# Optimization experiments

Hardware: AMD Instinct MI355X
Metric: run time of the kernel (lower is better)

## Reference

```python
import jax, jax.numpy as jnp
import numpy as np

HEADS = 8
EPS = 1e-5


def _quad_sums(a):
    """a: (B,h,H,W,...) -> (B,h,H,W,4,...) sums over the four inclusive
    quadrants [ :h+1,:w+1 | :h+1,w: | h:,:w+1 | h:,w: ] for every (h,w),
    via padded 2D prefix sums over axes (2,3)."""
    c = jnp.cumsum(jnp.cumsum(a, axis=2), axis=3)
    pads = [(0, 0)] * a.ndim
    pads[2] = (1, 0)
    pads[3] = (1, 0)
    P = jnp.pad(c, pads)  # P[...,i,j,...] = sum over rows<i, cols<j
    tl = P[:, :, 1:, 1:]
    tr = P[:, :, 1:, -1:] - P[:, :, 1:, :-1]
    bl = P[:, :, -1:, 1:] - P[:, :, :-1, 1:]
    br = P[:, :, -1:, -1:] - P[:, :, :-1, -1:] - P[:, :, -1:, :-1] + P[:, :, :-1, :-1]
    return jnp.stack([tl, tr, bl, br], axis=4)


def setup_inputs():
    key = jax.random.key(0)
    ks = jax.random.split(key, 12)
    B, H, W, D = 64, 48, 48, 64
    n = H * W
    hD = HEADS * D  # inner_dim = heads * dim_head, dim_head == dim
    rn = lambda k, shape: jax.random.normal(k, shape, dtype=jnp.float32) * 0.02
    return {
        "x": jax.random.normal(ks[0], (B, n, D), dtype=jnp.float32),
        "ln_g": jnp.ones((D,), jnp.float32),
        "ln_b": jnp.zeros((D,), jnp.float32),
        "Wqkv": rn(ks[1], (3 * hD, D)),
        "bqkv": jnp.zeros((3 * hD,), jnp.float32),
        "cls_tok": rn(ks[2], (D,)),
        "Wwqkv": rn(ks[3], (3 * D, D)),
        "bwqkv": jnp.zeros((3 * D,), jnp.float32),
        "Wwproj": rn(ks[4], (D, D)),
        "bwproj": jnp.zeros((D,), jnp.float32),
        "Wraq": rn(ks[5], (D, D)),
        "Wrak": rn(ks[6], (D, D)),
        "Wrav": rn(ks[7], (D, D)),
        "Wrao": rn(ks[8], (D, D)),
        "brao": jnp.zeros((D,), jnp.float32),
        "Wout": rn(ks[9], (D, hD)),
        "bout": jnp.zeros((D,), jnp.float32),
    }


def reference(x, ln_g, ln_b, Wqkv, bqkv, cls_tok, Wwqkv, bwqkv, Wwproj, bwproj,
              Wraq, Wrak, Wrav, Wrao, brao, Wout, bout):
    B, n, D = x.shape
    H = W = int(np.sqrt(n))
    h = HEADS
    hd = D // h                      # WindowAttention head dim
    scale_w = hd ** -0.5             # WindowAttention qk scale
    scale_ra = (D // h) ** -0.5      # RegionAggregator scale

    # LayerNorm (biased variance, as torch)
    mu = x.mean(-1, keepdims=True)
    var = ((x - mu) ** 2).mean(-1, keepdims=True)
    xn = (x - mu) / jnp.sqrt(var + EPS) * ln_g + ln_b

    # to_qkv: only q is consumed downstream (k, v are dead in the original forward)
    q = xn @ Wqkv[: h * D].T + bqkv[: h * D]
    q = q.reshape(B, n, h, D).transpose(0, 2, 1, 3)  # (B,h,n,D)  d == dim

    # WindowAttention: per-quadrant CLS-row attention, shared token keys/values.
    cls_qkv = (cls_tok @ Wwqkv.T + bwqkv).reshape(3, h, hd)
    q_c = cls_qkv[0] * scale_w                       # (h,hd) scaled cls query
    k_c, v_c = cls_qkv[1], cls_qkv[2]
    tok = (xn @ Wwqkv.T + bwqkv).reshape(B, n, 3, h, hd)
    k_t = tok[:, :, 1].transpose(0, 2, 1, 3)         # (B,h,n,hd)
    v_t = tok[:, :, 2].transpose(0, 2, 1, 3)
    logits = jnp.einsum('hd,bhnd->bhn', q_c, k_t)    # cls -> token logits
    cls_logit = jnp.einsum('hd,hd->h', q_c, k_c)     # cls -> cls logit
    m = jnp.maximum(logits.max(-1), cls_logit)       # (B,h) stabilizer
    e = jnp.exp(logits - m[..., None]).reshape(B, h, H, W)
    ecls = jnp.exp(cls_logit - m)                    # (B,h)
    ev = e[..., None] * v_t.reshape(B, h, H, W, hd)
    Se = _quad_sums(e)                               # (B,h,H,W,4)
    Sev = _quad_sums(ev)                             # (B,h,H,W,4,hd)
    denom = ecls[:, :, None, None, None] + Se
    num = ecls[:, :, None, None, None, None] * v_c[None, :, None, None, None, :] + Sev
    cls_out = num / denom[..., None]                 # (B,h,H,W,4,hd)
    cls_out = cls_out.transpose(0, 2, 3, 4, 1, 5).reshape(B, n, 4, D)
    regions = cls_out @ Wwproj.T + bwproj            # (B,n,4,D)

    # RegionAggregator (regions are identical across heads -> broadcast)
    qp = jnp.einsum('bhnd,ed->bhne', q, Wraq)
    kp = regions @ Wrak.T                            # (B,n,4,D)
    vp = regions @ Wrav.T
    scores = jnp.einsum('bhnd,bnrd->bhnr', qp, kp) * scale_ra
    attn = jax.nn.softmax(scores, axis=-1)
    agg = jnp.einsum('bhnr,bnrd->bhnd', attn, vp)
    out = agg @ Wrao.T + brao                        # (B,h,n,D)
    out = out.transpose(0, 2, 1, 3).reshape(B, n, h * D)
    return out @ Wout.T + bout                       # (B,n,D)
```

## Files before the change

kernel.cpp:

```cpp
#include <hip/hip_runtime.h>
#include <math.h>


#define SCALE_W  0.3535533905932738f
#define SCALE_RA 0.3535533905932738f
#define LN_EPS 1e-5f

typedef __attribute__((ext_vector_type(8))) short bf16x8;
typedef __attribute__((ext_vector_type(4))) float f32x4;

#define OFF_XN   0ull
#define SZ_XN    (64ull*2304*64)
#define OFF_KT   (OFF_XN + SZ_XN)
#define SZ_KT    (64ull*8*2304*8)
#define OFF_VT   (OFF_KT + SZ_KT)
#define OFF_PA   (OFF_VT + SZ_KT)
#define SZ_PA    (512ull*2401*5)
#define OFF_PB   (OFF_PA + SZ_PA)
#define SZ_PB    (512ull*2401*4)
#define OFF_ECLS (OFF_PB + SZ_PB)
#define OFF_QC   (OFF_ECLS + 512)
#define OFF_KC   (OFF_QC + 64)
#define OFF_VC   (OFF_KC + 64)
#define OFF_CLOG (OFF_VC + 64)
#define OFF_BK   (OFF_CLOG + 8)
#define OFF_BV   (OFF_BK + 64)
#define OFF_AH   (OFF_BV + 64)
#define OFF_W1   (OFF_AH + 512)
#define OFF_WZ   (OFF_W1 + 64)
#define OFF_B2   (OFF_WZ + 64)
#define OFF_V2   (OFF_B2 + 512)
#define OFF_UH   (OFF_V2 + 512)
#define OFF_CH   (OFF_UH + 512)
#define OFF_C1   (OFF_CH + 8)
#define OFF_G    (OFF_C1 + 64)
#define OFF_Z    (OFF_G + 32768)

__device__ inline void split2(float x, unsigned short &h, unsigned short &l) {
  unsigned u = __float_as_uint(x);
  unsigned hr = (u + 0x7fffu + ((u >> 16) & 1u)) >> 16;
  h = (unsigned short)hr;
  float hf = __uint_as_float(hr << 16);
  float lo = x - hf;
  unsigned u2 = __float_as_uint(lo);
  l = (unsigned short)((u2 + 0x7fffu + ((u2 >> 16) & 1u)) >> 16);
}

__device__ inline void split2x2(float x0, float x1, unsigned &h, unsigned &l) {
  asm("v_cvt_pk_bf16_f32 %0, %1, %2" : "=v"(h) : "v"(x0), "v"(x1));
  float r0 = x0 - __uint_as_float(h << 16);
  float r1 = x1 - __uint_as_float(h & 0xffff0000u);
  asm("v_cvt_pk_bf16_f32 %0, %1, %2" : "=v"(l) : "v"(r0), "v"(r1));
}

__device__ inline float dot64(const float* __restrict__ a, const float* __restrict__ b) {
  float s0 = 0.f, s1 = 0.f, s2 = 0.f, s3 = 0.f;
  #pragma unroll
  for (int d = 0; d < 64; d += 4) {
    float4 av = *(const float4*)(a + d);
    float4 bv = *(const float4*)(b + d);
    s0 += av.x * bv.x; s1 += av.y * bv.y;
    s2 += av.z * bv.z; s3 += av.w * bv.w;
  }
  return (s0 + s1) + (s2 + s3);
}

__global__ __launch_bounds__(256) void k_pre(const float* __restrict__ x,
      const float* __restrict__ ln_g, const float* __restrict__ ln_b,
      const float* __restrict__ Wqkv, const float* __restrict__ bqkv,
      const float* __restrict__ cls_tok, const float* __restrict__ Wwqkv,
      const float* __restrict__ bwqkv, const float* __restrict__ Wwproj,
      const float* __restrict__ bwproj, const float* __restrict__ Wraq,
      const float* __restrict__ Wrak, const float* __restrict__ Wrav,
      const float* __restrict__ Wrao, const float* __restrict__ brao,
      const float* __restrict__ Wout, const float* __restrict__ bout,
      float* __restrict__ ws) {
  __shared__ float smu[12928];
  int tid = threadIdx.x;
  int blk = blockIdx.x;

  if (blk < 2304) {
    float* xnT = smu;
    float* xt  = smu + 4352;
    float* wkv = smu + 4352;
    float* muL = smu + 4352 + 8448;
    float* rsL = muL + 64;

    long T0 = (long)blk * 64;
    int tok = tid >> 2, seg = tid & 3;

    const float4* x4 = (const float4*)(x + (T0 + tok)*64 + seg*16);
    float4 va = x4[0], vb = x4[1], vc4 = x4[2], vd = x4[3];
    {
      float* xp = xt + tok*65 + seg*16;
      xp[0]=va.x; xp[1]=va.y; xp[2]=va.z; xp[3]=va.w;
      xp[4]=vb.x; xp[5]=vb.y; xp[6]=vb.z; xp[7]=vb.w;
      xp[8]=vc4.x; xp[9]=vc4.y; xp[10]=vc4.z; xp[11]=vc4.w;
      xp[12]=vd.x; xp[13]=vd.y; xp[14]=vd.z; xp[15]=vd.w;
    }
    __syncthreads();
    if (tid < 64) {
      float s = 0.f;
      for (int i2 = 0; i2 < 64; ++i2) s += xt[tid*65 + i2];
      float mu = s * (1.0f/64.0f);
      float v = 0.f;
      for (int i2 = 0; i2 < 64; ++i2) { float d = xt[tid*65 + i2] - mu; v += d*d; }
      v *= (1.0f/64.0f);
      muL[tid] = mu; rsL[tid] = 1.0f / sqrtf(v + LN_EPS);
    }
    __syncthreads();
    {
      float mu = muL[tok], rs = rsL[tok];
      float xv[16];
      #pragma unroll
      for (int k = 0; k < 16; ++k) {
        int i2 = seg*16 + k;
        float v = (xt[tok*65 + i2] - mu) * rs * ln_g[i2] + ln_b[i2];
        xv[k] = v;
        xnT[i2*68 + tok] = v;
      }
      float4* xng = (float4*)(ws + OFF_XN + (T0 + tok)*64 + seg*16);
      xng[0] = make_float4(xv[0], xv[1], xv[2], xv[3]);
      xng[1] = make_float4(xv[4], xv[5], xv[6], xv[7]);
      xng[2] = make_float4(xv[8], xv[9], xv[10], xv[11]);
      xng[3] = make_float4(xv[12], xv[13], xv[14], xv[15]);
    }
    __syncthreads();
    {
      int o = tid >> 1, dh = (tid & 1) * 32;
      #pragma unroll
      for (int k = 0; k < 32; k += 4) {
        float4 w4 = *(const float4*)(Wwqkv + (64 + o)*64 + dh + k);
        wkv[(dh+k+0)*132 + o] = w4.x;
        wkv[(dh+k+1)*132 + o] = w4.y;
        wkv[(dh+k+2)*132 + o] = w4.z;
        wkv[(dh+k+3)*132 + o] = w4.w;
      }
    }
    __syncthreads();
    int tokq = tid & 15, og = tid >> 4;
    float acc[4][8];
    #pragma unroll
    for (int ti = 0; ti < 4; ++ti)
      #pragma unroll
      for (int k = 0; k < 8; ++k) acc[ti][k] = 0.f;
    for (int d2 = 0; d2 < 64; ++d2) {
      float4 a4 = *(float4*)&xnT[d2*68 + tokq*4];
      float4 b0 = *(float4*)&wkv[d2*132 + og*8];
      float4 b1 = *(float4*)&wkv[d2*132 + og*8 + 4];
      float aa[4] = {a4.x, a4.y, a4.z, a4.w};
      float bbv[8] = {b0.x,b0.y,b0.z,b0.w,b1.x,b1.y,b1.z,b1.w};
      #pragma unroll
      for (int ti = 0; ti < 4; ++ti)
        #pragma unroll
        for (int k = 0; k < 8; ++k) acc[ti][k] += aa[ti]*bbv[k];
    }
    int hh2 = og & 7;
    float bsv[8];
    #pragma unroll
    for (int k = 0; k < 8; ++k) bsv[k] = bwqkv[64 + og*8 + k];
    unsigned long long dstoff = (og < 8) ? OFF_KT : OFF_VT;
    #pragma unroll
    for (int ti = 0; ti < 4; ++ti) {
      long ntok = T0 + tokq*4 + ti;
      int bb = (int)(ntok / 2304);
      int nl = (int)(ntok % 2304);
      float* dst = ws + dstoff + ((long)(bb*8 + hh2)*2304 + nl)*8;
      *(float4*)dst = make_float4(acc[ti][0]+bsv[0], acc[ti][1]+bsv[1], acc[ti][2]+bsv[2], acc[ti][3]+bsv[3]);
      *(float4*)(dst+4) = make_float4(acc[ti][4]+bsv[4], acc[ti][5]+bsv[5], acc[ti][6]+bsv[6], acc[ti][7]+bsv[7]);
    }
  } else if (blk < 2320) {
    float* A  = smu;
    float* Bl = smu + 4160;
    int wblk = blk - 2304;
    if (wblk < 8) {
      int hh = wblk;
      for (int o = tid; o < 4096; o += 256) {
        int d = o & 63, e = o >> 6; float s = 0.f;
        for (int f = 0; f < 64; ++f) s += Wraq[f*64+d] * Wrak[f*64+e];
        A[d*65 + e] = s;
      }
      __syncthreads();
      for (int o = tid; o < 4096; o += 256) {
        int j = o & 63, i = o >> 6; float s = 0.f;
        for (int f = 0; f < 64; ++f) s += A[i*65 + f] * Wwproj[f*64 + j];
        Bl[i*65 + j] = s;
      }
      __syncthreads();
      unsigned short* gb = (unsigned short*)(ws + OFF_G) + hh*8192;
      for (int o = tid; o < 4096; o += 256) {
        int d = o & 63, e = o >> 6; float s = 0.f;
        for (int f = 0; f < 64; ++f) s += Wqkv[(hh*64+f)*64 + d] * Bl[f*65 + e];
        unsigned short h16, l16;
        split2(s, h16, l16);
        int base = (e >> 4)*2048 + (d >> 5)*1024 + (((d >> 3) & 3)*16 + (e & 15))*8 + (d & 7);
        gb[base]       = h16;
        gb[base + 512] = l16;
      }
    } else {
      int hh = wblk - 8;
      for (int o = tid; o < 4096; o += 256) {
        int d = o & 63, e = o >> 6; float s = 0.f;
        for (int f = 0; f < 64; ++f) s += Wrav[e*64+f] * Wwproj[f*64+d];
        A[e*65 + d] = s;
      }
      __syncthreads();
      for (int o = tid; o < 4096; o += 256) {
        int d = o & 63, i = o >> 6; float s = 0.f;
        for (int f = 0; f < 64; ++f) s += Wrao[i*64+f] * A[f*65 + d];
        Bl[i*65 + d] = s;
      }
      __syncthreads();
      unsigned short* zb = (unsigned short*)(ws + OFF_Z) + hh*8192;
      for (int o = tid; o < 4096; o += 256) {
        int d = o & 63, e = o >> 6; float s = 0.f;
        for (int f = 0; f < 64; ++f) s += Wout[e*512 + hh*64 + f] * Bl[f*65 + d];
        unsigned short h16, l16;
        split2(s, h16, l16);
        int base = (e >> 4)*2048 + (d >> 5)*1024 + (((d >> 3) & 3)*16 + (e & 15))*8 + (d & 7);
        zb[base]       = h16;
        zb[base + 512] = l16;
      }
    }
  } else {
    float* bwz = smu;
    for (int idx = tid; idx < 768; idx += 256) {
      if (idx < 192) {
        float s = bwqkv[idx] + dot64(Wwqkv + idx*64, cls_tok);
        if (idx < 64) ws[OFF_QC + idx] = s * SCALE_W;
        else if (idx < 128) ws[OFF_KC + idx - 64] = s;
        else ws[OFF_VC + idx - 128] = s;
      } else if (idx < 256) {
        int e = idx - 192;
        ws[OFF_BV + e] = dot64(Wrav + e*64, bwproj);
      } else {
        int t2 = idx - 256; int hh = t2 >> 6, e = t2 & 63;
        ws[OFF_AH + t2] = dot64(Wraq + e*64, bqkv + hh*64);
      }
    }
    __syncthreads();
    for (int idx = tid; idx < 584; idx += 256) {
      if (idx < 8) {
        float s = 0.f;
        for (int u = 0; u < 8; ++u) s += ws[OFF_QC + idx*8+u] * ws[OFF_KC + idx*8+u];
        ws[OFF_CLOG + idx] = s;
      } else if (idx < 72) {
        int e = idx - 8;
        ws[OFF_WZ + e] = dot64(Wrao + e*64, ws + OFF_BV);
      } else {
        int t2 = idx - 72; int hh = t2 >> 6, e = t2 & 63; float s = 0.f;
        for (int d = 0; d < 64; ++d) s += Wrak[d*64+e] * ws[OFF_AH + hh*64+d];
        ws[OFF_B2 + t2] = s;
      }
    }
    __syncthreads();
    if (tid < 64) bwz[tid] = brao[tid] + ws[OFF_WZ + tid];
    __syncthreads();
    for (int idx = tid; idx < 576; idx += 256) {
      if (idx < 512) {
        int hh = idx >> 6, e = idx & 63; float s = 0.f;
        for (int d = 0; d < 64; ++d) s += Wwproj[d*64+e] * ws[OFF_B2 + hh*64+d];
        ws[OFF_V2 + idx] = s;
      } else {
        int e = idx - 512;
        float s0 = 0.f, s1 = 0.f, s2 = 0.f, s3 = 0.f;
        for (int f = 0; f < 512; f += 4) {
          float4 w4 = *(const float4*)(Wout + e*512 + f);
          float4 b4 = *(const float4*)&bwz[f & 63];
          s0 += w4.x*b4.x; s1 += w4.y*b4.y; s2 += w4.z*b4.z; s3 += w4.w*b4.w;
        }
        ws[OFF_C1 + e] = bout[e] + (s0 + s1) + (s2 + s3);
      }
    }
  }
}

__global__ __launch_bounds__(512) void k_prefix(float* __restrict__ ws) {
  __shared__ float Pp[49*49*5];
  __shared__ float red[8];
  int tid = threadIdx.x;
  int blk = blockIdx.x;
  int g = blk & 1, bh = blk >> 1;
  int hh = bh & 7;
  const float* kt = ws + OFF_KT + (long)bh*2304*8;
  const float* vt = ws + OFF_VT + (long)bh*2304*8 + (g ? 4 : 0);
  float qc[8];
  #pragma unroll
  for (int u = 0; u < 8; ++u) qc[u] = ws[OFF_QC + hh*8 + u];
  float lgr[5];
  float mloc = -1e30f;
  #pragma unroll
  for (int it = 0; it < 5; ++it) {
    int nn = tid + it*512;
    if (nn < 2304) {
      const float4* kk = (const float4*)(kt + nn*8);
      float4 k0 = kk[0], k1 = kk[1];
      float lv = qc[0]*k0.x + qc[1]*k0.y + qc[2]*k0.z + qc[3]*k0.w
               + qc[4]*k1.x + qc[5]*k1.y + qc[6]*k1.z + qc[7]*k1.w;
      lgr[it] = lv;
      mloc = fmaxf(mloc, lv);
    }
  }
  #pragma unroll
  for (int mk = 1; mk < 64; mk <<= 1) mloc = fmaxf(mloc, __shfl_xor(mloc, mk, 64));
  if ((tid & 63) == 0) red[tid >> 6] = mloc;
  __syncthreads();
  float m = fmaxf(fmaxf(fmaxf(red[0], red[1]), fmaxf(red[2], red[3])),
                  fmaxf(fmaxf(red[4], red[5]), fmaxf(red[6], red[7])));
  m = fmaxf(m, ws[OFF_CLOG + hh]);
  if (tid == 0 && g == 0) ws[OFF_ECLS + bh] = __expf(ws[OFF_CLOG + hh] - m);
  #pragma unroll
  for (int it = 0; it < 5; ++it) {
    int nn = tid + it*512;
    if (nn < 2304) {
      int i2 = nn / 48, j2 = nn % 48;
      float ev = __expf(lgr[it] - m);
      float4 v4 = *(const float4*)(vt + nn*8);
      float* cell = &Pp[((i2+1)*49 + (j2+1))*5];
      if (g == 0) {
        cell[0] = ev; cell[1] = ev*v4.x; cell[2] = ev*v4.y; cell[3] = ev*v4.z; cell[4] = ev*v4.w;
      } else {
        cell[0] = ev*v4.x; cell[1] = ev*v4.y; cell[2] = ev*v4.z; cell[3] = ev*v4.w;
      }
    }
  }
  __syncthreads();
  int nc = g ? 4 : 5;
  if (tid < 48*nc) {
    int j2 = tid / nc + 1, c = tid % nc;
    float s = 0.f;
    for (int i0 = 1; i0 <= 48; i0 += 8) {
      float v[8];
      #pragma unroll
      for (int k = 0; k < 8; ++k) v[k] = Pp[((i0+k)*49 + j2)*5 + c];
      #pragma unroll
      for (int k = 0; k < 8; ++k) { s += v[k]; v[k] = s; }
      #pragma unroll
      for (int k = 0; k < 8; ++k) Pp[((i0+k)*49 + j2)*5 + c] = v[k];
    }
  }
  __syncthreads();
  if (tid < 48*nc) {
    int i2 = tid / nc + 1, c = tid % nc;
    float s = 0.f;
    for (int j0 = 1; j0 <= 48; j0 += 8) {
      float v[8];
      #pragma unroll
      for (int k = 0; k < 8; ++k) v[k] = Pp[(i2*49 + j0+k)*5 + c];
      #pragma unroll
      for (int k = 0; k < 8; ++k) { s += v[k]; v[k] = s; }
      #pragma unroll
      for (int k = 0; k < 8; ++k) Pp[(i2*49 + j0+k)*5 + c] = v[k];
    }
  }
  __syncthreads();
  if (g == 0) {
    float* pa = ws + OFF_PA + (long)bh*12005;
    for (int idx = tid; idx < 12005; idx += 512) {
      int cell = idx / 5;
      int ii = cell / 49, jj = cell % 49;
      pa[idx] = (ii && jj) ? Pp[idx] : 0.f;
    }
  } else {
    float* pb = ws + OFF_PB + (long)bh*9604;
    for (int idx = tid; idx < 9604; idx += 512) {
      int cell = idx >> 2, c = idx & 3;
      int ii = cell / 49, jj = cell % 49;
      pb[idx] = (ii && jj) ? Pp[cell*5 + c] : 0.f;
    }
  }
}

__global__ __launch_bounds__(128) void k_main(const float* __restrict__ ws,
                                              float* __restrict__ outp) {
  __shared__ __align__(16) unsigned short XNhi[16*64];
  __shared__ __align__(16) unsigned short XNlo[16*64];
  __shared__ __align__(16) unsigned short CBhi[16*128];
  __shared__ __align__(16) unsigned short CBlo[16*128];
  __shared__ __align__(16) float Tlds[16*128];

  int tid = threadIdx.x;
  int tok = tid >> 3, eg = tid & 7;
  int lane = tid & 63, wv = tid >> 6;
  int quad = lane >> 4, lrow = lane & 15;
  int wcol = wv;
  long T0 = (long)blockIdx.x * 16;
  int b = (int)(T0 / 2304);
  int n = (int)(T0 % 2304) + tok;
  int i2 = n / 48, j2 = n % 48;

  {
    const float4* p4 = (const float4*)(ws + OFF_XN + (T0 + tok)*64 + eg*8);
    float4 xa = p4[0], xb = p4[1];
    float xv[8] = {xa.x, xa.y, xa.z, xa.w, xb.x, xb.y, xb.z, xb.w};
    union { unsigned u[4]; uint2 d[2]; } ph, pl;
    #pragma unroll
    for (int k = 0; k < 8; k += 2) split2x2(xv[k], xv[k+1], ph.u[k>>1], pl.u[k>>1]);
    int off = tok*64 + ((eg*8) ^ ((tok & 7) << 3));
    *(uint2*)&XNhi[off]     = ph.d[0];
    *(uint2*)&XNhi[off + 4] = ph.d[1];
    *(uint2*)&XNlo[off]     = pl.d[0];
    *(uint2*)&XNlo[off + 4] = pl.d[1];
  }

  float cls0[8], cls1[8], cls2[8], cls3[8];
  {
    float ec = ws[OFF_ECLS + b*8 + eg];
    const float* PA = ws + OFF_PA + (long)(b*8 + eg)*12005;
    const float* PB = ws + OFF_PB + (long)(b*8 + eg)*9604;
    int c_ij  = i2*49 + j2;
    int c_ij1 = c_ij + 1;
    int c_iW  = i2*49 + 48;
    int c_1j  = c_ij + 49;
    int c_1j1 = c_1j + 1;
    int c_1W  = c_iW + 49;
    int c_Hj  = 48*49 + j2;
    int c_Hj1 = c_Hj + 1;
    int c_HW  = 48*49 + 48;
    float rden[4];
    {
      float tl = PA[c_1j1*5];
      float tr = PA[c_1W*5] - PA[c_1j*5];
      float bl = PA[c_Hj1*5] - PA[c_ij1*5];
      float br = PA[c_HW*5] - PA[c_iW*5] - PA[c_Hj*5] + PA[c_ij*5];
      rden[0] = 1.0f/(ec + tl); rden[1] = 1.0f/(ec + tr);
      rden[2] = 1.0f/(ec + bl); rden[3] = 1.0f/(ec + br);
    }
    #pragma unroll
    for (int u = 0; u < 4; ++u) {
      int c = 1 + u;
      float tl = PA[c_1j1*5 + c];
      float tr = PA[c_1W*5 + c] - PA[c_1j*5 + c];
      float bl = PA[c_Hj1*5 + c] - PA[c_ij1*5 + c];
      float br = PA[c_HW*5 + c] - PA[c_iW*5 + c] - PA[c_Hj*5 + c] + PA[c_ij*5 + c];
      float nv = ec * ws[OFF_VC + eg*8 + u];
      cls0[u] = (nv + tl) * rden[0];
      cls1[u] = (nv + tr) * rden[1];
      cls2[u] = (nv + bl) * rden[2];
      cls3[u] = (nv + br) * rden[3];
    }
    #pragma unroll
    for (int u = 4; u < 8; ++u) {
      int c = u - 4;
      float tl = PB[c_1j1*4 + c];
      float tr = PB[c_1W*4 + c] - PB[c_1j*4 + c];
      float bl = PB[c_Hj1*4 + c] - PB[c_ij1*4 + c];
      float br = PB[c_HW*4 + c] - PB[c_iW*4 + c] - PB[c_Hj*4 + c] + PB[c_ij*4 + c];
      float nv = ec * ws[OFF_VC + eg*8 + u];
      cls0[u] = (nv + tl) * rden[0];
      cls1[u] = (nv + tr) * rden[1];
      cls2[u] = (nv + bl) * rden[2];
      cls3[u] = (nv + br) * rden[3];
    }
  }
  __syncthreads();

  const unsigned short* gball = (const unsigned short*)(ws + OFF_G);
  const unsigned short* zball = (const unsigned short*)(ws + OFF_Z);

  f32x4 oa0 = {0.f,0.f,0.f,0.f};
  f32x4 oa1 = {0.f,0.f,0.f,0.f};

  int rr = lrow;
  int sw3 = (rr & 7) << 3;
  const unsigned short* arh = XNhi + rr*64;
  const unsigned short* arl = XNlo + rr*64;
  const unsigned short* crh = CBhi + rr*128;
  const unsigned short* crl = CBlo + rr*128;

  for (int it = 0; it < 4; ++it) {
    int h0 = it*2;
    {
      union { bf16x8 v; uint2 d[2]; } ah0, ah1, al0, al1;
      int oa = (quad*8) ^ sw3;
      int ob = (32 + quad*8) ^ sw3;
      ah0.d[0] = *(const uint2*)(arh + oa); ah0.d[1] = *(const uint2*)(arh + oa + 4);
      ah1.d[0] = *(const uint2*)(arh + ob); ah1.d[1] = *(const uint2*)(arh + ob + 4);
      al0.d[0] = *(const uint2*)(arl + oa); al0.d[1] = *(const uint2*)(arl + oa + 4);
      al1.d[0] = *(const uint2*)(arl + ob); al1.d[1] = *(const uint2*)(arl + ob + 4);
      #pragma unroll
      for (int c = 0; c < 4; ++c) {
        int colb = wcol*4 + c;
        int e0 = colb*16 + lrow;
        const unsigned short* gh = gball + (h0 + (colb >> 2))*8192 + (colb & 3)*2048 + lane*8;
        bf16x8 bh0 = *(const bf16x8*)(gh);
        bf16x8 bl0 = *(const bf16x8*)(gh + 512);
        bf16x8 bh1 = *(const bf16x8*)(gh + 1024);
        bf16x8 bl1 = *(const bf16x8*)(gh + 1536);
        f32x4 acc = {0.f,0.f,0.f,0.f};
        acc = __builtin_amdgcn_mfma_f32_16x16x32_bf16(ah0.v, bh0, acc, 0, 0, 0);
        acc = __builtin_amdgcn_mfma_f32_16x16x32_bf16(ah1.v, bh1, acc, 0, 0, 0);
        acc = __builtin_amdgcn_mfma_f32_16x16x32_bf16(al0.v, bh0, acc, 0, 0, 0);
        acc = __builtin_amdgcn_mfma_f32_16x16x32_bf16(al1.v, bh1, acc, 0, 0, 0);
        acc = __builtin_amdgcn_mfma_f32_16x16x32_bf16(ah0.v, bl0, acc, 0, 0, 0);
        acc = __builtin_amdgcn_mfma_f32_16x16x32_bf16(ah1.v, bl1, acc, 0, 0, 0);
        float v2v = ws[OFF_V2 + h0*64 + e0];
        #pragma unroll
        for (int r = 0; r < 4; ++r) {
          int trow = quad*4 + r;
          Tlds[trow*128 + (e0 ^ ((trow & 7) << 2))] = acc[r] + v2v;
        }
      }
    }
    __syncthreads();
    {
      float tv0[8], tv1[8];
      {
        int base = tok*128;
        int sw2 = (tok & 7) << 2;
        float4 a0 = *(const float4*)&Tlds[base + ((eg*8) ^ sw2)];
        float4 b0 = *(const float4*)&Tlds[base + ((eg*8 + 4) ^ sw2)];
        float4 a1 = *(const float4*)&Tlds[base + ((64 + eg*8) ^ sw2)];
        float4 b1 = *(const float4*)&Tlds[base + ((64 + eg*8 + 4) ^ sw2)];
        tv0[0]=a0.x; tv0[1]=a0.y; tv0[2]=a0.z; tv0[3]=a0.w;
        tv0[4]=b0.x; tv0[5]=b0.y; tv0[6]=b0.z; tv0[7]=b0.w;
        tv1[0]=a1.x; tv1[1]=a1.y; tv1[2]=a1.z; tv1[3]=a1.w;
        tv1[4]=b1.x; tv1[5]=b1.y; tv1[6]=b1.z; tv1[7]=b1.w;
      }
      float p0=0.f,p1=0.f,p2=0.f,p3=0.f,q0=0.f,q1=0.f,q2=0.f,q3=0.f;
      #pragma unroll
      for (int k = 0; k < 8; ++k) {
        p0 += tv0[k]*cls0[k]; p1 += tv0[k]*cls1[k];
        p2 += tv0[k]*cls2[k]; p3 += tv0[k]*cls3[k];
        q0 += tv1[k]*cls0[k]; q1 += tv1[k]*cls1[k];
        q2 += tv1[k]*cls2[k]; q3 += tv1[k]*cls3[k];
      }
      #pragma unroll
      for (int mk = 1; mk < 8; mk <<= 1) {
        p0 += __shfl_xor(p0, mk, 8); p1 += __shfl_xor(p1, mk, 8);
        p2 += __shfl_xor(p2, mk, 8); p3 += __shfl_xor(p3, mk, 8);
        q0 += __shfl_xor(q0, mk, 8); q1 += __shfl_xor(q1, mk, 8);
        q2 += __shfl_xor(q2, mk, 8); q3 += __shfl_xor(q3, mk, 8);
      }
      union { unsigned u[4]; uint2 d[2]; } ch, cl;
      int cbBase = tok*128;
      int swc = (tok & 7) << 3;
      {
        float s0 = p0*SCALE_RA, s1 = p1*SCALE_RA, s2 = p2*SCALE_RA, s3 = p3*SCALE_RA;
        float mm = fmaxf(fmaxf(s0, s1), fmaxf(s2, s3));
        float e0 = __expf(s0-mm), e1 = __expf(s1-mm), e2 = __expf(s2-mm), e3 = __expf(s3-mm);
        float inv = 1.0f/(e0+e1+e2+e3);
        float av0 = e0*inv, av1 = e1*inv, av2 = e2*inv, av3 = e3*inv;
        #pragma unroll
        for (int k = 0; k < 8; k += 2) {
          float cv0 = av0*cls0[k] + av1*cls1[k] + av2*cls2[k] + av3*cls3[k];
          float cv1 = av0*cls0[k+1] + av1*cls1[k+1] + av2*cls2[k+1] + av3*cls3[k+1];
          split2x2(cv0, cv1, ch.u[k>>1], cl.u[k>>1]);
        }
        int o = cbBase + ((eg*8) ^ swc);
        *(uint2*)&CBhi[o]     = ch.d[0]; *(uint2*)&CBhi[o + 4] = ch.d[1];
        *(uint2*)&CBlo[o]     = cl.d[0]; *(uint2*)&CBlo[o + 4] = cl.d[1];
      }
      {
        float s0 = q0*SCALE_RA, s1 = q1*SCALE_RA, s2 = q2*SCALE_RA, s3 = q3*SCALE_RA;
        float mm = fmaxf(fmaxf(s0, s1), fmaxf(s2, s3));
        float e0 = __expf(s0-mm), e1 = __expf(s1-mm), e2 = __expf(s2-mm), e3 = __expf(s3-mm);
        float inv = 1.0f/(e0+e1+e2+e3);
        float av0 = e0*inv, av1 = e1*inv, av2 = e2*inv, av3 = e3*inv;
        #pragma unroll
        for (int k = 0; k < 8; k += 2) {
          float cv0 = av0*cls0[k] + av1*cls1[k] + av2*cls2[k] + av3*cls3[k];
          float cv1 = av0*cls0[k+1] + av1*cls1[k+1] + av2*cls2[k+1] + av3*cls3[k+1];
          split2x2(cv0, cv1, ch.u[k>>1], cl.u[k>>1]);
        }
        int o = cbBase + ((64 + eg*8) ^ swc);
        *(uint2*)&CBhi[o]     = ch.d[0]; *(uint2*)&CBhi[o + 4] = ch.d[1];
        *(uint2*)&CBlo[o]     = cl.d[0]; *(uint2*)&CBlo[o + 4] = cl.d[1];
      }
    }
    __syncthreads();
    {
      #pragma unroll
      for (int c = 0; c < 2; ++c) {
        int colb = wcol*2 + c;
        int e0 = colb*16 + lrow;
        f32x4 acc = (c == 0) ? oa0 : oa1;
        #pragma unroll
        for (int kb = 0; kb < 4; ++kb) {
          union { bf16x8 v; uint2 d[2]; } ah, al;
          int o = (kb*32 + quad*8) ^ sw3;
          ah.d[0] = *(const uint2*)(crh + o); ah.d[1] = *(const uint2*)(crh + o + 4);
          al.d[0] = *(const uint2*)(crl + o); al.d[1] = *(const uint2*)(crl + o + 4);
          const unsigned short* zc = zball + (h0 + (kb >> 1))*8192 + colb*2048 + (kb & 1)*1024 + lane*8;
          bf16x8 bh = *(const bf16x8*)(zc);
          bf16x8 bl = *(const bf16x8*)(zc + 512);
          acc = __builtin_amdgcn_mfma_f32_16x16x32_bf16(ah.v, bh, acc, 0, 0, 0);
          acc = __builtin_amdgcn_mfma_f32_16x16x32_bf16(al.v, bh, acc, 0, 0, 0);
          acc = __builtin_amdgcn_mfma_f32_16x16x32_bf16(ah.v, bl, acc, 0, 0, 0);
        }
        if (c == 0) oa0 = acc; else oa1 = acc;
      }
    }
  }
  #pragma unroll
  for (int c = 0; c < 2; ++c) {
    int e0 = (wcol*2 + c)*16 + lrow;
    float cov = ws[OFF_C1 + e0];
    f32x4 oa = (c == 0) ? oa0 : oa1;
    #pragma unroll
    for (int r = 0; r < 4; ++r)
      outp[(T0 + quad*4 + r)*64 + e0] = oa[r] + cov;
  }
}

extern "C" void kernel_launch(void* const* d_in, const int* in_sizes, int n_in,
                              void* d_out, int out_size, void* d_ws, size_t ws_size,
                              hipStream_t stream) {
  const float* x      = (const float*)d_in[0];
  const float* ln_g   = (const float*)d_in[1];
  const float* ln_b   = (const float*)d_in[2];
  const float* Wqkv   = (const float*)d_in[3];
  const float* bqkv   = (const float*)d_in[4];
  const float* cls_tok= (const float*)d_in[5];
  const float* Wwqkv  = (const float*)d_in[6];
  const float* bwqkv  = (const float*)d_in[7];
  const float* Wwproj = (const float*)d_in[8];
  const float* bwproj = (const float*)d_in[9];
  const float* Wraq   = (const float*)d_in[10];
  const float* Wrak   = (const float*)d_in[11];
  const float* Wrav   = (const float*)d_in[12];
  const float* Wrao   = (const float*)d_in[13];
  const float* brao   = (const float*)d_in[14];
  const float* Wout   = (const float*)d_in[15];
  const float* bout   = (const float*)d_in[16];
  float* ws = (float*)d_ws;
  float* outp = (float*)d_out;

  hipLaunchKernelGGL(k_pre, dim3(2321), dim3(256), 0, stream,
                     x, ln_g, ln_b, Wqkv, bqkv, cls_tok, Wwqkv, bwqkv,
                     Wwproj, bwproj, Wraq, Wrak, Wrav, Wrao, brao, Wout, bout, ws);
  hipLaunchKernelGGL(k_prefix, dim3(1024), dim3(512), 0, stream, ws);
  hipLaunchKernelGGL(k_main, dim3(9216), dim3(128), 0, stream, ws, outp);
}
```

Baseline: 360.9 us.

## Merge prefix-sum block pairs and schedule weight-prep blocks first in k_pre

k_prefix used to launch two blocks per (batch, head), and each one recomputed the logits, max and exponentials. It now launches one block that computes them once and runs two passes through the shared-memory prefix-sum buffer: first e with ev[0..3], then ev[4..7]. k_pre block indices are remapped so the small weight-precompute blocks come first and no longer trail behind the 2304 token blocks. The cost is half as many k_prefix blocks, each with more serial work and extra barriers, which lowers parallelism on a large GPU.

```diff
diff --git a/kernel.cpp b/kernel.cpp
--- a/kernel.cpp
+++ b/kernel.cpp
@@ -79,14 +79,14 @@
   int tid = threadIdx.x;
   int blk = blockIdx.x;
 
-  if (blk < 2304) {
+  if (blk >= 17) {
     float* xnT = smu;
     float* xt  = smu + 4352;
     float* wkv = smu + 4352;
     float* muL = smu + 4352 + 8448;
     float* rsL = muL + 64;
 
-    long T0 = (long)blk * 64;
+    long T0 = (long)(blk - 17) * 64;
     int tok = tid >> 2, seg = tid & 3;
 
     const float4* x4 = (const float4*)(x + (T0 + tok)*64 + seg*16);
@@ -169,10 +169,10 @@
       *(float4*)dst = make_float4(acc[ti][0]+bsv[0], acc[ti][1]+bsv[1], acc[ti][2]+bsv[2], acc[ti][3]+bsv[3]);
       *(float4*)(dst+4) = make_float4(acc[ti][4]+bsv[4], acc[ti][5]+bsv[5], acc[ti][6]+bsv[6], acc[ti][7]+bsv[7]);
     }
-  } else if (blk < 2320) {
+  } else if (blk >= 1) {
     float* A  = smu;
     float* Bl = smu + 4160;
-    int wblk = blk - 2304;
+    int wblk = blk - 1;
     if (wblk < 8) {
       int hh = wblk;
       for (int o = tid; o < 4096; o += 256) {
@@ -279,15 +279,14 @@
   __shared__ float Pp[49*49*5];
   __shared__ float red[8];
   int tid = threadIdx.x;
-  int blk = blockIdx.x;
-  int g = blk & 1, bh = blk >> 1;
+  int bh = blockIdx.x;
   int hh = bh & 7;
   const float* kt = ws + OFF_KT + (long)bh*2304*8;
-  const float* vt = ws + OFF_VT + (long)bh*2304*8 + (g ? 4 : 0);
+  const float* vt = ws + OFF_VT + (long)bh*2304*8;
   float qc[8];
   #pragma unroll
   for (int u = 0; u < 8; ++u) qc[u] = ws[OFF_QC + hh*8 + u];
-  float lgr[5];
+  float ev[5];
   float mloc = -1e30f;
   #pragma unroll
   for (int it = 0; it < 5; ++it) {
@@ -297,7 +296,7 @@
       float4 k0 = kk[0], k1 = kk[1];
       float lv = qc[0]*k0.x + qc[1]*k0.y + qc[2]*k0.z + qc[3]*k0.w
                + qc[4]*k1.x + qc[5]*k1.y + qc[6]*k1.z + qc[7]*k1.w;
-      lgr[it] = lv;
+      ev[it] = lv;
       mloc = fmaxf(mloc, lv);
     }
   }
@@ -308,26 +307,26 @@
   float m = fmaxf(fmaxf(fmaxf(red[0], red[1]), fmaxf(red[2], red[3])),
                   fmaxf(fmaxf(red[4], red[5]), fmaxf(red[6], red[7])));
   m = fmaxf(m, ws[OFF_CLOG + hh]);
-  if (tid == 0 && g == 0) ws[OFF_ECLS + bh] = __expf(ws[OFF_CLOG + hh] - m);
+  if (tid == 0) ws[OFF_ECLS + bh] = __expf(ws[OFF_CLOG + hh] - m);
+  #pragma unroll
+  for (int it = 0; it < 5; ++it) {
+    int nn = tid + it*512;
+    if (nn < 2304) ev[it] = __expf(ev[it] - m);
+  }
   #pragma unroll
   for (int it = 0; it < 5; ++it) {
     int nn = tid + it*512;
     if (nn < 2304) {
       int i2 = nn / 48, j2 = nn % 48;
-      float ev = __expf(lgr[it] - m);
       float4 v4 = *(const float4*)(vt + nn*8);
       float* cell = &Pp[((i2+1)*49 + (j2+1))*5];
-      if (g == 0) {
-        cell[0] = ev; cell[1] = ev*v4.x; cell[2] = ev*v4.y; cell[3] = ev*v4.z; cell[4] = ev*v4.w;
-      } else {
-        cell[0] = ev*v4.x; cell[1] = ev*v4.y; cell[2] = ev*v4.z; cell[3] = ev*v4.w;
-      }
-    }
-  }
-  __syncthreads();
-  int nc = g ? 4 : 5;
-  if (tid < 48*nc) {
-    int j2 = tid / nc + 1, c = tid % nc;
+      float e0 = ev[it];
+      cell[0] = e0; cell[1] = e0*v4.x; cell[2] = e0*v4.y; cell[3] = e0*v4.z; cell[4] = e0*v4.w;
+    }
+  }
+  __syncthreads();
+  if (tid < 240) {
+    int j2 = tid / 5 + 1, c = tid % 5;
     float s = 0.f;
     for (int i0 = 1; i0 <= 48; i0 += 8) {
       float v[8];
@@ -340,8 +339,8 @@
     }
   }
   __syncthreads();
-  if (tid < 48*nc) {
-    int i2 = tid / nc + 1, c = tid % nc;
+  if (tid < 240) {
+    int i2 = tid / 5 + 1, c = tid % 5;
     float s = 0.f;
     for (int j0 = 1; j0 <= 48; j0 += 8) {
       float v[8];
@@ -354,14 +353,56 @@
     }
   }
   __syncthreads();
-  if (g == 0) {
+  {
     float* pa = ws + OFF_PA + (long)bh*12005;
     for (int idx = tid; idx < 12005; idx += 512) {
       int cell = idx / 5;
       int ii = cell / 49, jj = cell % 49;
       pa[idx] = (ii && jj) ? Pp[idx] : 0.f;
     }
-  } else {
+  }
+  __syncthreads();
+  #pragma unroll
+  for (int it = 0; it < 5; ++it) {
+    int nn = tid + it*512;
+    if (nn < 2304) {
+      int i2 = nn / 48, j2 = nn % 48;
+      float4 v4 = *(const float4*)(vt + nn*8 + 4);
+      float* cell = &Pp[((i2+1)*49 + (j2+1))*5];
+      float e0 = ev[it];
+      cell[0] = e0*v4.x; cell[1] = e0*v4.y; cell[2] = e0*v4.z; cell[3] = e0*v4.w;
+    }
+  }
+  __syncthreads();
+  if (tid < 192) {
+    int j2 = tid >> 2, c = tid & 3; j2 += 1;
+    float s = 0.f;
+    for (int i0 = 1; i0 <= 48; i0 += 8) {
+      float v[8];
+      #pragma unroll
+      for (int k = 0; k < 8; ++k) v[k] = Pp[((i0+k)*49 + j2)*5 + c];
+      #pragma unroll
+      for (int k = 0; k < 8; ++k) { s += v[k]; v[k] = s; }
+      #pragma unroll
+      for (int k = 0; k < 8; ++k) Pp[((i0+k)*49 + j2)*5 + c] = v[k];
+    }
+  }
+  __syncthreads();
+  if (tid < 192) {
+    int i2 = tid >> 2, c = tid & 3; i2 += 1;
+    float s = 0.f;
+    for (int j0 = 1; j0 <= 48; j0 += 8) {
+      float v[8];
+      #pragma unroll
+      for (int k = 0; k < 8; ++k) v[k] = Pp[(i2*49 + j0+k)*5 + c];
+      #pragma unroll
+      for (int k = 0; k < 8; ++k) { s += v[k]; v[k] = s; }
+      #pragma unroll
+      for (int k = 0; k < 8; ++k) Pp[(i2*49 + j0+k)*5 + c] = v[k];
+    }
+  }
+  __syncthreads();
+  {
     float* pb = ws + OFF_PB + (long)bh*9604;
     for (int idx = tid; idx < 9604; idx += 512) {
       int cell = idx >> 2, c = idx & 3;
@@ -629,6 +670,6 @@
   hipLaunchKernelGGL(k_pre, dim3(2321), dim3(256), 0, stream,
                      x, ln_g, ln_b, Wqkv, bqkv, cls_tok, Wwqkv, bwqkv,
                      Wwproj, bwproj, Wraq, Wrak, Wrav, Wrao, brao, Wout, bout, ws);
-  hipLaunchKernelGGL(k_prefix, dim3(1024), dim3(512), 0, stream, ws);
+  hipLaunchKernelGGL(k_prefix, dim3(512), dim3(512), 0, stream, ws);
   hipLaunchKernelGGL(k_main, dim3(9216), dim3(128), 0, stream, ws, outp);
 }
```

Result: faster. 338.6 us (-6.2%).
